# Kernel optimization log

Hardware: AMD Instinct MI355X
Metric: run time of the kernel (lower is better)

The kernel has to match this reference:

```python
import jax, jax.numpy as jnp
import numpy as np

B, C_IN, H, W = 32, 64, 64, 64
D, O, S_SP, K = 256, 512, 4, 3


def setup_inputs() -> dict:
    key = jax.random.key(0)
    k1, k2, k3, k4, k5 = jax.random.split(key, 5)
    x = jax.random.normal(k1, (B, C_IN, H, W), dtype=jnp.float32)
    dictionary = jax.random.normal(k2, (D, C_IN, K, K), dtype=jnp.float32)
    lookup_coefficients = jax.random.normal(k3, (O, S_SP), dtype=jnp.float32)
    bias = jax.random.normal(k4, (O,), dtype=jnp.float32)
    lookup_indices = jax.random.randint(k5, (O, S_SP), 0, D)
    return {
        "x": x,
        "dictionary": dictionary,
        "lookup_coefficients": lookup_coefficients,
        "bias": bias,
        "lookup_indices": lookup_indices,
    }


def reference(x, dictionary, lookup_coefficients, bias, lookup_indices):
    # Dictionary conv: S has shape [B, D, H, W] (stride 1, padding 1, 3x3 kernel)
    S = jax.lax.conv_general_dilated(
        x, dictionary,
        window_strides=(1, 1),
        padding=((1, 1), (1, 1)),
        dimension_numbers=("NCHW", "OIHW", "NCHW"),
    )
    # Build dense [O, D] combine matrix via scatter-add (duplicate indices
    # accumulate, matching the original += loop), then one GEMM.
    rows = jnp.arange(O)[:, None]  # [O, 1] broadcast against [O, sparsity]
    Wc = jnp.zeros((O, D), dtype=S.dtype).at[rows, lookup_indices].add(lookup_coefficients)
    out = jnp.einsum("bdhw,od->bohw", S, Wc)
    return out + bias[None, :, None, None]
```

## Files before the change

kernel.cpp:

```cpp
#include <hip/hip_runtime.h>
#include <stdint.h>

#define NB 32
#define NC 64
#define NH 64
#define NW 64
#define NO 512
#define ND 256
#define HP 66

typedef __bf16 bf16x8 __attribute__((ext_vector_type(8)));
typedef short  s16x8  __attribute__((ext_vector_type(8)));
typedef float  f32x4  __attribute__((ext_vector_type(4)));
typedef uint32_t u32x2 __attribute__((ext_vector_type(2)));

__device__ __forceinline__ uint16_t f2bf(float f) {
  uint32_t u = __builtin_bit_cast(uint32_t, f);
  u += 0x7fffu + ((u >> 16) & 1u);
  return (uint16_t)(u >> 16);
}
__device__ __forceinline__ uint32_t pk2(float a, float b) {
  return (uint32_t)f2bf(a) | ((uint32_t)f2bf(b) << 16);
}
__device__ __forceinline__ float ubf_lo(uint32_t u) {
  return __builtin_bit_cast(float, u << 16);
}
__device__ __forceinline__ float ubf_hi(uint32_t u) {
  return __builtin_bit_cast(float, u & 0xffff0000u);
}

__device__ __forceinline__ void gld16(const uint16_t* g, uint16_t* l) {
  __builtin_amdgcn_global_load_lds(
      (const __attribute__((address_space(1))) void*)(g),
      (__attribute__((address_space(3))) void*)(l), 16, 0, 0);
}

__global__ void k_prep(const float* __restrict__ dict,
                       const float* __restrict__ x,
                       uint16_t*    __restrict__ Wd,
                       uint16_t*    __restrict__ xh) {
  const int bid = blockIdx.x;
  const int t = threadIdx.x;
  if (bid < ND) {
    const int d = bid;
#pragma unroll
    for (int j = 0; j < 3; ++j) {
      const int id = t + j * 256;
      if (id < 576) {
        const int c = id & 63, p = id >> 6;
        Wd[(size_t)(p * ND + d) * 64 + c] = f2bf(dict[d * 576 + c * 9 + p]);
      }
    }
    return;
  }
  const int bh = bid - ND;
  const int b = bh / HP, hp = bh % HP;
  uint16_t* row = xh + (size_t)(b * HP + hp) * 4096;
  int4* r4 = reinterpret_cast<int4*>(row);
  if (hp == 0 || hp == HP - 1) {
    r4[t]       = int4{0, 0, 0, 0};
    r4[t + 256] = int4{0, 0, 0, 0};
    return;
  }
  __shared__ float tile[64][65];
  const int h = hp - 1;
  const int w = t & 63;
#pragma unroll
  for (int c = (t >> 6); c < 64; c += 4)
    tile[c][w] = x[((size_t)(b * NC + c) * NH + h) * NW + w];
  __syncthreads();
#pragma unroll
  for (int i = 0; i < 2; ++i) {
    const int s = t + i * 256;
    const int w2 = s >> 3, cb = s & 7;
    uint32_t dd[4];
#pragma unroll
    for (int j = 0; j < 4; ++j)
      dd[j] = pk2(tile[cb * 8 + 2 * j][w2], tile[cb * 8 + 2 * j + 1][w2]);
    r4[w2 * 8 + (cb ^ (w2 & 7))] =
        int4{(int)dd[0], (int)dd[1], (int)dd[2], (int)dd[3]};
  }
}

__global__ __launch_bounds__(512, 2) void k_conv(
    const uint16_t* __restrict__ xh,
    const uint16_t* __restrict__ Wd,
    const float*    __restrict__ coef,
    const int*      __restrict__ idx,
    const float*    __restrict__ bias,
    float*          __restrict__ out) {
  __shared__ __align__(16) uint16_t smem[65536];
  uint16_t* xs = smem;
  uint8_t*  Sb = (uint8_t*)smem;

  const int t = threadIdx.x;
  const int lane = t & 63;
  const int wid  = t >> 6;
  const int flat = blockIdx.x;
  const int s    = (flat & 7) * 64 + (flat >> 3);
  const int b    = s >> 4;
  const int hq   = s & 15;
  const int h0p  = hq * 4;

  if (t < 96) {
    const int r = t >> 4, sl = (t >> 3) & 1, j = t & 7;
    reinterpret_cast<int4*>(xs)[r * 528 + sl * 520 + j] = int4{0, 0, 0, 0};
  }
  {
#pragma unroll
    for (int j = 0; j < 6; ++j) {
      const int ch = wid * 6 + j;
      const int r = ch >> 3, k = ch & 7;
      gld16(xh + (size_t)(b * HP + h0p + r) * 4096 + k * 512 + lane * 8,
            xs + r * 4224 + 64 + k * 512);
    }
  }

  const int wd  = wid & 3;
  const int wn  = wid >> 2;
  const int l15 = lane & 15;
  const int lg  = lane >> 4;

  const uint16_t* wbase = Wd + (size_t)(wd * 64 + l15) * 64 + lg * 8;

  f32x4 acc[8][4];
#pragma unroll
  for (int pb = 0; pb < 8; ++pb)
#pragma unroll
    for (int db = 0; db < 4; ++db)
      acc[pb][db] = (f32x4){0.f, 0.f, 0.f, 0.f};

  __syncthreads();

#pragma unroll
  for (int g = 0; g < 3; ++g) {
    const int dw = g - 1;
#pragma unroll
    for (int q = 0; q < 2; ++q) {
      const int cbB = (q * 4 + lg) ^ ((l15 + dw) & 7);
      const uint16_t* xb = xs + (l15 + dw + 1) * 64 + cbB * 8;
      bf16x8 braw[4][4];
#pragma unroll
      for (int rr = 0; rr < 4; ++rr)
#pragma unroll
        for (int nw = 0; nw < 4; ++nw)
          braw[rr][nw] = __builtin_bit_cast(bf16x8,
              *reinterpret_cast<const s16x8*>(
                  xb + (wn * 2 + rr) * 4224 + nw * 1024));
#pragma unroll
      for (int dh = 0; dh < 3; ++dh) {
        const int tap = dh * 3 + g;
        bf16x8 af[4];
#pragma unroll
        for (int db = 0; db < 4; ++db)
          af[db] = __builtin_bit_cast(bf16x8,
              *reinterpret_cast<const s16x8*>(
                  wbase + (size_t)tap * 16384 + db * 1024 + q * 32));
#pragma unroll
        for (int pb = 0; pb < 8; ++pb)
#pragma unroll
          for (int db = 0; db < 4; ++db)
            acc[pb][db] = __builtin_amdgcn_mfma_f32_16x16x32_bf16(
                braw[(pb >> 2) + dh][pb & 3], af[db], acc[pb][db], 0, 0, 0);
      }
    }
  }

  __syncthreads();
#pragma unroll
  for (int pb = 0; pb < 8; ++pb) {
#pragma unroll
    for (int db = 0; db < 4; ++db) {
      const int d   = wd * 64 + db * 16 + l15;
      const int pix = (wn * 2 + (pb >> 2)) * 64 + (pb & 3) * 16 + lg * 4;
      u32x2 u;
      u[0] = pk2(acc[pb][db][0], acc[pb][db][1]);
      u[1] = pk2(acc[pb][db][2], acc[pb][db][3]);
      *reinterpret_cast<u32x2*>(
          Sb + d * 512 + ((pix * 2) ^ ((d & 7) << 4))) = u;
    }
  }
  __syncthreads();

  const int hrow = lane >> 4;
  const int wcol = (lane & 15) * 4;
#pragma unroll 4
  for (int oo = 0; oo < 64; ++oo) {
    const int o = wid * 64 + oo;
    const int4 iv = *reinterpret_cast<const int4*>(idx + o * 4);
    const f32x4 cv = *reinterpret_cast<const f32x4*>(coef + o * 4);
    const float bv = bias[o];
    f32x4 v = {bv, bv, bv, bv};
#define GATH(ROW, CS) do {                                                  \
      const int r_ = (ROW);                                                 \
      const u32x2 u_ = *reinterpret_cast<const u32x2*>(                     \
          Sb + r_ * 512 + ((lane * 8) ^ ((r_ & 7) << 4)));                  \
      const float c_ = (CS);                                                \
      v[0] += c_ * ubf_lo(u_[0]);  v[1] += c_ * ubf_hi(u_[0]);              \
      v[2] += c_ * ubf_lo(u_[1]);  v[3] += c_ * ubf_hi(u_[1]);              \
    } while (0)
    GATH(iv.x, cv[0]);
    GATH(iv.y, cv[1]);
    GATH(iv.z, cv[2]);
    GATH(iv.w, cv[3]);
#undef GATH
    float* dst = out + ((size_t)(b * NO + o) * NH + hq * 4 + hrow) * NW + wcol;
    __builtin_nontemporal_store(v, reinterpret_cast<f32x4*>(dst));
  }
}

extern "C" void kernel_launch(void* const* d_in, const int* in_sizes, int n_in,
                              void* d_out, int out_size, void* d_ws, size_t ws_size,
                              hipStream_t stream) {
  const float* x    = (const float*)d_in[0];
  const float* dict = (const float*)d_in[1];
  const float* coef = (const float*)d_in[2];
  const float* bias = (const float*)d_in[3];
  const int*   idx  = (const int*)d_in[4];
  float* out = (float*)d_out;

  uint16_t* xh = (uint16_t*)d_ws;
  uint16_t* Wd = (uint16_t*)((char*)d_ws + (18u << 20));

  hipLaunchKernelGGL(k_prep, dim3(ND + NB * HP), dim3(256), 0, stream,
                     dict, x, Wd, xh);
  hipLaunchKernelGGL(k_conv, dim3(512), dim3(512), 0, stream,
                     xh, Wd, coef, idx, bias, out);
}
```

Before: 102.6 us.

## Halve per-block output rows to raise occupancy and double grid size

Each conv block now covers 2 output rows instead of 4. Shared memory is halved to 64KB, the accumulator array shrinks from 8x4 to 4x4, and launch bounds request 4 blocks per CU, with 1024 blocks in the grid. The aim is better latency hiding and more even load balance across the 256 CUs. In exchange, input-row halo reuse drops (4 rows loaded per 2 output rows, versus 6 per 4). Each weight fragment also feeds fewer MFMAs, so weight loads from global/L2 per FLOP roughly double, and the final stores are narrower 8-byte writes.

```diff
diff --git a/kernel.cpp b/kernel.cpp
--- a/kernel.cpp
+++ b/kernel.cpp
@@ -12,6 +12,7 @@
 typedef __bf16 bf16x8 __attribute__((ext_vector_type(8)));
 typedef short  s16x8  __attribute__((ext_vector_type(8)));
 typedef float  f32x4  __attribute__((ext_vector_type(4)));
+typedef float  f32x2  __attribute__((ext_vector_type(2)));
 typedef uint32_t u32x2 __attribute__((ext_vector_type(2)));
 
 __device__ __forceinline__ uint16_t f2bf(float f) {
@@ -82,14 +83,14 @@
   }
 }
 
-__global__ __launch_bounds__(512, 2) void k_conv(
+__global__ __launch_bounds__(512, 4) void k_conv(
     const uint16_t* __restrict__ xh,
     const uint16_t* __restrict__ Wd,
     const float*    __restrict__ coef,
     const int*      __restrict__ idx,
     const float*    __restrict__ bias,
     float*          __restrict__ out) {
-  __shared__ __align__(16) uint16_t smem[65536];
+  __shared__ __align__(16) uint16_t smem[32768];
   uint16_t* xs = smem;
   uint8_t*  Sb = (uint8_t*)smem;
 
@@ -97,21 +98,21 @@
   const int lane = t & 63;
   const int wid  = t >> 6;
   const int flat = blockIdx.x;
-  const int s    = (flat & 7) * 64 + (flat >> 3);
-  const int b    = s >> 4;
-  const int hq   = s & 15;
-  const int h0p  = hq * 4;
-
-  if (t < 96) {
+  const int s    = (flat & 7) * 128 + (flat >> 3);
+  const int b    = s >> 5;
+  const int ht   = s & 31;
+  const int h0   = ht * 2;
+
+  if (t < 64) {
     const int r = t >> 4, sl = (t >> 3) & 1, j = t & 7;
     reinterpret_cast<int4*>(xs)[r * 528 + sl * 520 + j] = int4{0, 0, 0, 0};
   }
   {
 #pragma unroll
-    for (int j = 0; j < 6; ++j) {
-      const int ch = wid * 6 + j;
+    for (int j = 0; j < 4; ++j) {
+      const int ch = wid * 4 + j;
       const int r = ch >> 3, k = ch & 7;
-      gld16(xh + (size_t)(b * HP + h0p + r) * 4096 + k * 512 + lane * 8,
+      gld16(xh + (size_t)(b * HP + h0 + r) * 4096 + k * 512 + lane * 8,
             xs + r * 4224 + 64 + k * 512);
     }
   }
@@ -123,9 +124,9 @@
 
   const uint16_t* wbase = Wd + (size_t)(wd * 64 + l15) * 64 + lg * 8;
 
-  f32x4 acc[8][4];
-#pragma unroll
-  for (int pb = 0; pb < 8; ++pb)
+  f32x4 acc[4][4];
+#pragma unroll
+  for (int pb = 0; pb < 4; ++pb)
 #pragma unroll
     for (int db = 0; db < 4; ++db)
       acc[pb][db] = (f32x4){0.f, 0.f, 0.f, 0.f};
@@ -139,73 +140,69 @@
     for (int q = 0; q < 2; ++q) {
       const int cbB = (q * 4 + lg) ^ ((l15 + dw) & 7);
       const uint16_t* xb = xs + (l15 + dw + 1) * 64 + cbB * 8;
-      bf16x8 braw[4][4];
-#pragma unroll
-      for (int rr = 0; rr < 4; ++rr)
-#pragma unroll
-        for (int nw = 0; nw < 4; ++nw)
-          braw[rr][nw] = __builtin_bit_cast(bf16x8,
-              *reinterpret_cast<const s16x8*>(
-                  xb + (wn * 2 + rr) * 4224 + nw * 1024));
 #pragma unroll
       for (int dh = 0; dh < 3; ++dh) {
         const int tap = dh * 3 + g;
-        bf16x8 af[4];
+        bf16x8 braw[4], af[4];
+#pragma unroll
+        for (int nw = 0; nw < 4; ++nw)
+          braw[nw] = __builtin_bit_cast(bf16x8,
+              *reinterpret_cast<const s16x8*>(
+                  xb + (wn + dh) * 4224 + nw * 1024));
 #pragma unroll
         for (int db = 0; db < 4; ++db)
           af[db] = __builtin_bit_cast(bf16x8,
               *reinterpret_cast<const s16x8*>(
                   wbase + (size_t)tap * 16384 + db * 1024 + q * 32));
 #pragma unroll
-        for (int pb = 0; pb < 8; ++pb)
+        for (int pb = 0; pb < 4; ++pb)
 #pragma unroll
           for (int db = 0; db < 4; ++db)
             acc[pb][db] = __builtin_amdgcn_mfma_f32_16x16x32_bf16(
-                braw[(pb >> 2) + dh][pb & 3], af[db], acc[pb][db], 0, 0, 0);
+                braw[pb], af[db], acc[pb][db], 0, 0, 0);
       }
     }
   }
 
   __syncthreads();
 #pragma unroll
-  for (int pb = 0; pb < 8; ++pb) {
+  for (int pb = 0; pb < 4; ++pb) {
 #pragma unroll
     for (int db = 0; db < 4; ++db) {
       const int d   = wd * 64 + db * 16 + l15;
-      const int pix = (wn * 2 + (pb >> 2)) * 64 + (pb & 3) * 16 + lg * 4;
+      const int pix = wn * 64 + pb * 16 + lg * 4;
       u32x2 u;
       u[0] = pk2(acc[pb][db][0], acc[pb][db][1]);
       u[1] = pk2(acc[pb][db][2], acc[pb][db][3]);
       *reinterpret_cast<u32x2*>(
-          Sb + d * 512 + ((pix * 2) ^ ((d & 7) << 4))) = u;
-    }
-  }
-  __syncthreads();
-
-  const int hrow = lane >> 4;
-  const int wcol = (lane & 15) * 4;
+          Sb + d * 256 + ((pix * 2) ^ ((d & 7) << 5))) = u;
+    }
+  }
+  __syncthreads();
+
+  const int hrow = lane >> 5;
+  const int wcol = (lane & 31) * 2;
 #pragma unroll 4
   for (int oo = 0; oo < 64; ++oo) {
     const int o = wid * 64 + oo;
     const int4 iv = *reinterpret_cast<const int4*>(idx + o * 4);
     const f32x4 cv = *reinterpret_cast<const f32x4*>(coef + o * 4);
     const float bv = bias[o];
-    f32x4 v = {bv, bv, bv, bv};
+    f32x2 v = {bv, bv};
 #define GATH(ROW, CS) do {                                                  \
       const int r_ = (ROW);                                                 \
-      const u32x2 u_ = *reinterpret_cast<const u32x2*>(                     \
-          Sb + r_ * 512 + ((lane * 8) ^ ((r_ & 7) << 4)));                  \
+      const uint32_t u_ = *reinterpret_cast<const uint32_t*>(               \
+          Sb + r_ * 256 + ((lane * 4) ^ ((r_ & 7) << 5)));                  \
       const float c_ = (CS);                                                \
-      v[0] += c_ * ubf_lo(u_[0]);  v[1] += c_ * ubf_hi(u_[0]);              \
-      v[2] += c_ * ubf_lo(u_[1]);  v[3] += c_ * ubf_hi(u_[1]);              \
+      v[0] += c_ * ubf_lo(u_);  v[1] += c_ * ubf_hi(u_);                    \
     } while (0)
     GATH(iv.x, cv[0]);
     GATH(iv.y, cv[1]);
     GATH(iv.z, cv[2]);
     GATH(iv.w, cv[3]);
 #undef GATH
-    float* dst = out + ((size_t)(b * NO + o) * NH + hq * 4 + hrow) * NW + wcol;
-    __builtin_nontemporal_store(v, reinterpret_cast<f32x4*>(dst));
+    float* dst = out + ((size_t)(b * NO + o) * NH + h0 + hrow) * NW + wcol;
+    __builtin_nontemporal_store(v, reinterpret_cast<f32x2*>(dst));
   }
 }
 
@@ -224,6 +221,6 @@
 
   hipLaunchKernelGGL(k_prep, dim3(ND + NB * HP), dim3(256), 0, stream,
                      dict, x, Wd, xh);
-  hipLaunchKernelGGL(k_conv, dim3(512), dim3(512), 0, stream,
+  hipLaunchKernelGGL(k_conv, dim3(1024), dim3(512), 0, stream,
                      xh, Wd, coef, idx, bias, out);
 }
```

After: 133.0 us. 29.6% more time.
